# Kernel optimization log

Hardware: AMD Instinct MI355X
Metric: run time of the kernel (lower is better)

## Reference

```python
import jax, jax.numpy as jnp
import numpy as np

T, B, D = 2048, 4, 1024


def setup_inputs() -> dict:
    key = jax.random.key(0)
    ks = jax.random.split(key, 4)
    data = jax.random.normal(ks[0], (T, B, D), dtype=jnp.float32)
    W_qkv = jax.random.normal(ks[1], (D, 3 * D), dtype=jnp.float32) * 0.02
    b_qkv = jnp.zeros((3 * D,), dtype=jnp.float32)
    # torch stores pos_bias as [1,1,T,T]; bilinear interp to the same [T,T] size
    # (align_corners=False) is the identity, so we keep a [T,T] table directly.
    pos_bias_param = jax.random.normal(ks[2], (T, T), dtype=jnp.float32) * 0.02
    W_out = jax.random.normal(ks[3], (D, D), dtype=jnp.float32) * 0.02
    b_out = jnp.zeros((D,), dtype=jnp.float32)
    return {"data": data, "W_qkv": W_qkv, "b_qkv": b_qkv,
            "pos_bias_param": pos_bias_param, "W_out": W_out, "b_out": b_out}


def reference(data, W_qkv, b_qkv, pos_bias_param, W_out, b_out):
    # data: [T, B, D]
    qkv = data @ W_qkv + b_qkv                      # [T, B, 3D]
    q, k, v = jnp.split(qkv, 3, axis=-1)            # each [T, B, D]
    pb = pos_bias_param                             # [T, T] (i=query pos, j=key pos)
    max_key = jnp.max(k, axis=0, keepdims=True)     # [1, B, D]
    max_pb = jnp.max(pb, axis=1, keepdims=True)     # [T, 1]
    exp_key = jnp.exp(k - max_key)                  # [T, B, D]
    exp_pb = jnp.exp(pb - max_pb)                   # [T, T]
    # torch einsum 'ijb,jbd->ibd' with b=1 on pos_bias broadcasts -> plain ij contraction
    num = jnp.einsum('ij,jbd->ibd', exp_pb, exp_key * v)  # [T, B, D]
    den = jnp.einsum('ij,jbd->ibd', exp_pb, exp_key)       # [T, B, D]
    y = jax.nn.sigmoid(q) * num / den               # [T, B, D]
    return y @ W_out + b_out
```

## Files before the change

### kernel.cpp

```cpp
#include <hip/hip_runtime.h>
#include <stdint.h>

typedef unsigned short ushort_t;
typedef signed char s8;
typedef __attribute__((ext_vector_type(8))) short short8;
typedef __attribute__((ext_vector_type(4))) int int4v;
typedef __attribute__((ext_vector_type(4))) float float4v;

typedef const void __attribute__((address_space(1)))* gptr1_t;
typedef void __attribute__((address_space(3)))* lptr3_t;

#define SX   (5.5f/127.f)
#define ISX  (127.f/5.5f)
#define SW1  (0.11f/127.f)
#define ISW1 (127.f/0.11f)
#define S1   (SX*SW1)

static __device__ __forceinline__ ushort_t f2bf(float f) {
  unsigned u = __builtin_bit_cast(unsigned, f);
  u += 0x7fffu + ((u >> 16) & 1u);
  return (ushort_t)(u >> 16);
}
static __device__ __forceinline__ float bf2f(ushort_t h) {
  unsigned u = ((unsigned)h) << 16;
  return __builtin_bit_cast(float, u);
}
static __device__ __forceinline__ float frcp(float x) { return __builtin_amdgcn_rcpf(x); }
static __device__ __forceinline__ int q8(float x, float inv_s) {
  float v = fminf(fmaxf(x * inv_s, -127.f), 127.f);
  return (int)rintf(v);
}

__global__ __launch_bounds__(256)
void prep1(const float* __restrict__ data, s8* __restrict__ Xq,
           const float* __restrict__ Wqkv, s8* __restrict__ WqT) {
  __shared__ float t[32][33];
  const int blk = blockIdx.x, tid = threadIdx.x;
  if (blk < 8192) {
    int row = blk;
    int orow = (row & 3) * 2048 + (row >> 2);
    float4v v = ((const float4v*)(data + (size_t)row * 1024))[tid];
    int a0 = q8(v[0], ISX), a1 = q8(v[1], ISX), a2 = q8(v[2], ISX), a3 = q8(v[3], ISX);
    uint32_t p = (a0 & 255) | ((a1 & 255) << 8) | ((a2 & 255) << 16) | ((a3 & 255) << 24);
    ((uint32_t*)(Xq + (size_t)orow * 1024))[tid] = p;
  } else {
    int l = blk - 8192;
    int bx = l % 96, by = l / 96;
    int tx = tid & 31, ty = tid >> 5;
    int c = bx * 32 + tx;
    #pragma unroll
    for (int i = ty; i < 32; i += 8)
      t[i][tx] = Wqkv[(size_t)(by * 32 + i) * 3072 + c];
    __syncthreads();
    int r = by * 32 + tx;
    #pragma unroll
    for (int i = ty; i < 32; i += 8) {
      int orow = bx * 32 + i;
      orow = (orow < 1024) ? orow
           : (orow < 2048) ? 1024 + 2 * (orow - 1024)
                           : 1024 + 2 * (orow - 2048) + 1;
      WqT[(size_t)orow * 1024 + r] = (s8)q8(t[tx][i], ISW1);
    }
  }
}


#define FENCE() asm volatile("" ::: "memory")
#define BARRIER() do { FENCE(); __builtin_amdgcn_s_barrier(); FENCE(); } while (0)
#define SB() __builtin_amdgcn_sched_barrier(0)
#define WAIT_LGKM0() do { asm volatile("s_waitcnt lgkmcnt(0)" ::: "memory"); SB(); } while (0)
#define WAIT_LGKM8() do { asm volatile("s_waitcnt lgkmcnt(8)" ::: "memory"); SB(); } while (0)
#define WAIT_VM0()   do { asm volatile("s_waitcnt vmcnt(0)"   ::: "memory"); SB(); } while (0)

#define GLD(g, l) __builtin_amdgcn_global_load_lds((gptr1_t)(const void*)(g), \
                                                   (lptr3_t)(void*)(l), 16, 0, 0)

#define STAGEA(h, u, bb) do { \
  const char* gs_ = gA + (size_t)(h) * 128 * AROWB + (size_t)(u) * 128; \
  char* ls_ = Als + (bb) * 32768 + (((h) * 128 + wid * 16) << 7); \
  GLD(gs_, ls_); GLD(gs_ + 8 * AROWB, ls_ + 1024); \
} while (0)
#define STAGEB(h, u, bb) do { \
  const char* gs_ = gB + (size_t)(h) * 128 * BROWB + (size_t)(u) * 128; \
  char* ls_ = Bls + (bb) * 32768 + (((h) * 128 + wid * 16) << 7); \
  GLD(gs_, ls_); GLD(gs_ + 8 * BROWB, ls_ + 1024); \
} while (0)

#define STAGE4(gbase, lbase, tn, bb, ROWB) do { \
  const char* gs_ = (gbase) + (size_t)(tn) * 128; \
  char* ls_ = (lbase) + (bb) * 32768 + ((wid * 32) << 7); \
  GLD(gs_, ls_); GLD(gs_ + 8 * (size_t)(ROWB), ls_ + 1024); \
  GLD(gs_ + 16 * (size_t)(ROWB), ls_ + 2048); GLD(gs_ + 24 * (size_t)(ROWB), ls_ + 3072); \
} while (0)

#define LDA2(DST, p, bb) do { \
  const fragt* As_ = (const fragt*)(Als + (bb) * 32768); \
  _Pragma("unroll") \
  for (int ii_ = 0; ii_ < 2; ++ii_) { \
    const int row_ = arow + ((p) * 2 + ii_) * 16 + m16; \
    DST[ii_][0] = As_[row_ * 8 + (quad ^ swr)]; \
    DST[ii_][1] = As_[row_ * 8 + ((4 + quad) ^ swr)]; \
  } \
} while (0)
#define LDB2Q(DST, q, bb) do { \
  const fragt* Bs_ = (const fragt*)(Bls + (bb) * BSTRIDE); \
  _Pragma("unroll") \
  for (int jj_ = 0; jj_ < 2; ++jj_) { \
    const int row_ = brow + ((q) * 2 + jj_) * 16 + m16; \
    DST[jj_][0] = Bs_[row_ * 8 + (quad ^ swr)]; \
    DST[jj_][1] = Bs_[row_ * 8 + ((4 + quad) ^ swr)]; \
  } \
} while (0)

#define MM8(AF, BF, ib, jb) do { \
  __builtin_amdgcn_s_setprio(1); \
  _Pragma("unroll") \
  for (int ks_ = 0; ks_ < 2; ++ks_) \
    _Pragma("unroll") \
    for (int ii_ = 0; ii_ < 2; ++ii_) \
      _Pragma("unroll") \
      for (int jj_ = 0; jj_ < 2; ++jj_) \
        acc[(ib) + ii_][(jb) + jj_] = MFMA_OP( \
            AF[ii_][ks_], BF[jj_][ks_], acc[(ib) + ii_][(jb) + jj_]); \
  __builtin_amdgcn_s_setprio(0); \
  SB(); \
} while (0)

#define WAIT_LGKM4() do { asm volatile("s_waitcnt lgkmcnt(4)" ::: "memory"); SB(); } while (0)
#define TILE256_BODY(bb) \
  LDA2(afX, 0, bb); LDB2Q(bfQ0, 0, bb); SB(); \
  LDA2(afY, 1, bb); LDB2Q(bfQ1, 1, bb); SB(); \
  WAIT_LGKM8(); \
  MM8(afX, bfQ0, 0, 0); \
  WAIT_LGKM0(); \
  MM8(afX, bfQ1, 0, 2); \
  LDA2(afX, 2, bb); SB(); \
  MM8(afY, bfQ0, 2, 0); \
  MM8(afY, bfQ1, 2, 2); \
  LDA2(afY, 3, bb); SB(); \
  WAIT_LGKM4(); \
  MM8(afX, bfQ0, 4, 0); \
  MM8(afX, bfQ1, 4, 2); \
  WAIT_LGKM0(); \
  MM8(afY, bfQ0, 6, 0); \
  MM8(afY, bfQ1, 6, 2);

#define TILE256(bb, tn) do { \
  STAGEA(0, tn, (bb) ^ 1); STAGEA(1, tn, (bb) ^ 1); \
  STAGEB(0, tn, (bb) ^ 1); STAGEB(1, tn, (bb) ^ 1); \
  TILE256_BODY(bb) \
  WAIT_VM0(); \
  BARRIER(); \
} while (0)

#define TILE256_LAST(bb) do { TILE256_BODY(bb) } while (0)

#define MFMA_OP(a, b, c) __builtin_amdgcn_mfma_i32_16x16x64_i8(a, b, c, 0, 0, 0)
#define BSTRIDE 32768
__global__ __launch_bounds__(512, 2)
void g1mix(const s8* __restrict__ WqT, const s8* __restrict__ Xq,
           const float* __restrict__ bqkv,
           uint32_t* __restrict__ qP, ushort_t* __restrict__ GT,
           const float* __restrict__ pb, ushort_t* __restrict__ Pb,
           const float* __restrict__ Wout, ushort_t* __restrict__ WoT) {
  __shared__ __align__(16) char smem[131072];
  const int blk = blockIdx.x, tid = threadIdx.x;
  if (blk < 384) {
    typedef int4v fragt;
    const int wid  = tid >> 6;
    const int lane = tid & 63;
    const int wr = wid >> 2, wc = wid & 3;
    const int m16 = lane & 15, quad = lane >> 4;
    const int swr = m16 & 7;
    const int srow = lane >> 3, schk = lane & 7;
    const int arow = wr * 128, brow = wc * 64;

    const int wg = (blk & 7) * 48 + (blk >> 3);
    const int m0 = (wg >> 5) * 256;
    const int n0 = (wg & 31) * 256;

    int4v acc[8][4];
    #pragma unroll
    for (int i = 0; i < 8; ++i)
      #pragma unroll
      for (int j = 0; j < 4; ++j)
        #pragma unroll
        for (int r = 0; r < 4; ++r) acc[i][j][r] = 0;

    fragt afX[2][2], afY[2][2], bfQ0[2][2], bfQ1[2][2];

    const size_t AROWB = 1024, BROWB = 1024;
    const int colb = (schk ^ srow) * 16;
    const char* gA = (const char*)WqT + (size_t)(m0 + wid * 16 + srow) * 1024 + colb;
    const char* gB = (const char*)Xq  + (size_t)(n0 + wid * 16 + srow) * 1024 + colb;
    char* Als = smem;
    char* Bls = smem + 65536;

    STAGEA(0, 0, 0); STAGEA(1, 0, 0); STAGEB(0, 0, 0); STAGEB(1, 0, 0);
    WAIT_VM0();
    BARRIER();

    #pragma unroll 1
    for (int I = 0; I < 3; ++I) {
      TILE256(0, 2 * I + 1);
      TILE256(1, 2 * I + 2);
    }
    TILE256(0, 7);
    TILE256_LAST(1);

    if (m0 < 1024) {
      #pragma unroll
      for (int i = 0; i < 8; ++i)
        #pragma unroll
        for (int j = 0; j < 4; ++j) {
          const int gm = m0 + wr * 128 + i * 16 + quad * 4;
          const int gn = n0 + wc * 64 + j * 16 + m16;
          float f0 = (float)acc[i][j][0] * S1 + bqkv[gm];
          float f1 = (float)acc[i][j][1] * S1 + bqkv[gm + 1];
          float f2 = (float)acc[i][j][2] * S1 + bqkv[gm + 2];
          float f3 = (float)acc[i][j][3] * S1 + bqkv[gm + 3];
          qP[(size_t)(gm >> 1) * 8192 + gn]       = (uint32_t)f2bf(f0) | ((uint32_t)f2bf(f1) << 16);
          qP[(size_t)((gm >> 1) + 1) * 8192 + gn] = (uint32_t)f2bf(f2) | ((uint32_t)f2bf(f3) << 16);
        }
    } else {
      #pragma unroll
      for (int i = 0; i < 8; ++i)
        #pragma unroll
        for (int j = 0; j < 4; ++j) {
          const int gm = m0 + wr * 128 + i * 16 + quad * 4;
          const int gn = n0 + wc * 64 + j * 16 + m16;
          const int d  = (gm - 1024) >> 1;
          const int t  = gn & 2047, bb = gn >> 11;
          #pragma unroll
          for (int p = 0; p < 2; ++p) {
            float kk = (float)acc[i][j][2 * p]     * S1 + bqkv[1024 + d + p];
            float vv = (float)acc[i][j][2 * p + 1] * S1 + bqkv[2048 + d + p];
            float ek = __expf(kk);
            int c = bb * 1024 + d + p;
            GT[(size_t)(2 * c)     * 2048 + t] = f2bf(ek * vv);
            GT[(size_t)(2 * c + 1) * 2048 + t] = f2bf(ek);
          }
        }
    }
  } else if (blk < 640) {
    const int base = (blk - 384) * 4096;
    #pragma unroll
    for (int r = 0; r < 8; ++r) {
      int i = base + r * 512 + tid;
      float4v v = *(const float4v*)(pb + (size_t)i * 4);
      ushort_t o0 = f2bf(__expf(v[0])), o1 = f2bf(__expf(v[1]));
      ushort_t o2 = f2bf(__expf(v[2])), o3 = f2bf(__expf(v[3]));
      uint64_t p = (uint64_t)o0 | ((uint64_t)o1 << 16) | ((uint64_t)o2 << 32) | ((uint64_t)o3 << 48);
      *(uint64_t*)(Pb + (size_t)i * 4) = p;
    }
  } else {
    float (*t)[33] = (float (*)[33])smem;
    const int tx = tid & 31, ty = tid >> 5;
    #pragma unroll 1
    for (int rep = 0; rep < 8; ++rep) {
      int l = (blk - 640) * 8 + rep;
      int bx = l & 31, by = l >> 5;
      int c = bx * 32 + tx;
      #pragma unroll
      for (int i = ty; i < 32; i += 16)
        t[i][tx] = Wout[(size_t)(by * 32 + i) * 1024 + c];
      __syncthreads();
      int r = by * 32 + tx;
      #pragma unroll
      for (int i = ty; i < 32; i += 16)
        WoT[(size_t)(bx * 32 + i) * 1024 + r] = f2bf(t[tx][i]);
      __syncthreads();
    }
  }
}
#undef MFMA_OP
#undef BSTRIDE

#define MFMA_OP(a, b, c) __builtin_amdgcn_mfma_f32_16x16x32_bf16(a, b, c, 0, 0, 0)
#define BSTRIDE 16384
#define G3_STAGEB(tn, bb) do { \
  const char* gs_ = gB + (size_t)(tn) * 128; \
  char* ls_ = Bls + (bb) * 16384 + ((wid * 16) << 7); \
  GLD(gs_, ls_); GLD(gs_ + 8 * 2048, ls_ + 1024); \
} while (0)

#define G3_BODY(bb) \
  LDA2(afX, 0, bb); LDB2Q(bfQ0, 0, bb); SB(); \
  LDA2(afY, 1, bb); LDB2Q(bfQ1, 1, bb); SB(); \
  WAIT_LGKM8(); \
  MM8(afX, bfQ0, 0, 0); \
  WAIT_LGKM0(); \
  MM8(afX, bfQ1, 0, 2); \
  MM8(afY, bfQ0, 2, 0); \
  MM8(afY, bfQ1, 2, 2);

#define G3_TILE(bb, tn) do { \
  STAGE4(gA, Als, tn, (bb) ^ 1, 2048); \
  G3_STAGEB(tn, (bb) ^ 1); \
  G3_BODY(bb) \
  WAIT_VM0(); \
  BARRIER(); \
} while (0)

__global__ __launch_bounds__(512, 2)
void gemm3(const ushort_t* __restrict__ A, const ushort_t* __restrict__ BT,
           const float* __restrict__ bias, float* __restrict__ Cf) {
  __shared__ __align__(16) char smem[98304];
  typedef short8 fragt;
  const int tid  = threadIdx.x;
  const int wid  = tid >> 6;
  const int lane = tid & 63;
  const int wr = wid >> 1, wc = wid & 1;
  const int m16 = lane & 15, quad = lane >> 4;
  const int swr = m16 & 7;
  const int srow = lane >> 3, schk = lane & 7;
  const int arow = wr * 64, brow = wc * 64;

  const int bid = blockIdx.x;
  const int wg = (bid & 7) * 32 + (bid >> 3);
  const int m0 = (wg >> 3) * 256;
  const int n0 = (wg & 7) * 128;

  float4v acc[4][4];
  #pragma unroll
  for (int i = 0; i < 4; ++i)
    #pragma unroll
    for (int j = 0; j < 4; ++j)
      #pragma unroll
      for (int r = 0; r < 4; ++r) acc[i][j][r] = 0.0f;

  fragt afX[2][2], afY[2][2], bfQ0[2][2], bfQ1[2][2];

  const int colb = (schk ^ srow) * 16;
  const char* gA = (const char*)A  + (size_t)(m0 + wid * 32 + srow) * 2048 + colb;
  const char* gB = (const char*)BT + (size_t)(n0 + wid * 16 + srow) * 2048 + colb;
  char* Als = smem;
  char* Bls = smem + 65536;

  STAGE4(gA, Als, 0, 0, 2048);
  G3_STAGEB(0, 0);
  WAIT_VM0();
  BARRIER();

  #pragma unroll 1
  for (int I = 0; I < 7; ++I) {
    G3_TILE(0, 2 * I + 1);
    G3_TILE(1, 2 * I + 2);
  }
  G3_TILE(0, 15);
  G3_BODY(1)

  #pragma unroll
  for (int i = 0; i < 4; ++i)
    #pragma unroll
    for (int j = 0; j < 4; ++j) {
      const int gm = m0 + wr * 64 + i * 16 + quad * 4;
      const int gn = n0 + wc * 64 + j * 16 + m16;
      const float bv = bias[gn];
      #pragma unroll
      for (int r = 0; r < 4; ++r)
        Cf[(size_t)(gm + r) * 1024 + gn] = acc[i][j][r] + bv;
    }
}
#undef MFMA_OP
#undef BSTRIDE

#define MFMA_OP(a, b, c) __builtin_amdgcn_mfma_f32_16x16x32_bf16(a, b, c, 0, 0, 0)
#define BSTRIDE 32768
__global__ __launch_bounds__(512, 2)
void aft256(const ushort_t* __restrict__ A, const ushort_t* __restrict__ BT,
            ushort_t* __restrict__ Yb, const uint32_t* __restrict__ qP) {
  __shared__ __align__(16) char smem[131072];
  typedef short8 fragt;
  const int tid  = threadIdx.x;
  const int wid  = tid >> 6;
  const int lane = tid & 63;
  const int wr = wid >> 2, wc = wid & 3;
  const int m16 = lane & 15, quad = lane >> 4;
  const int swr = m16 & 7;
  const int srow = lane >> 3, schk = lane & 7;
  const int arow = wr * 128, brow = wc * 64;

  const int bid = blockIdx.x;
  const int wg = (bid & 7) * 32 + (bid >> 3);
  const int m0 = (wg >> 3) * 256;
  const int n0 = (wg & 7) * 256;

  float4v acc[8][4];
  #pragma unroll
  for (int i = 0; i < 8; ++i)
    #pragma unroll
    for (int j = 0; j < 4; ++j)
      #pragma unroll
      for (int r = 0; r < 4; ++r) acc[i][j][r] = 0.0f;

  fragt afX[2][2], afY[2][2], bfQ0[2][2], bfQ1[2][2];

  const size_t AROWB = 4096, BROWB = 4096;
  const int colb = (schk ^ srow) * 16;
  const char* gA = (const char*)A  + (size_t)(m0 + wid * 16 + srow) * 4096 + colb;
  const char* gB = (const char*)BT + (size_t)(n0 + wid * 16 + srow) * 4096 + colb;
  char* Als = smem;
  char* Bls = smem + 65536;

  STAGEA(0, 0, 0); STAGEA(1, 0, 0); STAGEB(0, 0, 0); STAGEB(1, 0, 0);
  WAIT_VM0();
  BARRIER();

  #pragma unroll 1
  for (int I = 0; I < 15; ++I) {
    TILE256(0, 2 * I + 1);
    TILE256(1, 2 * I + 2);
  }
  TILE256(0, 31);
  TILE256_LAST(1);

  __syncthreads();

  uint32_t* tb = (uint32_t*)smem;
  const int cbase = m0 >> 1;
  const int b = cbase >> 10, dbase = cbase & 1023;
  const int pbase = dbase >> 1;
  #pragma unroll
  for (int i = 0; i < 8; ++i) {
    const int wl = wr * 32 + i * 4 + quad;
    #pragma unroll
    for (int j = 0; j < 4; ++j) {
      const int tl = wc * 64 + j * 16 + m16;
      const int t  = n0 + tl;
      uint32_t qw = qP[(size_t)(pbase + wl) * 8192 + b * 2048 + t];
      float q0 = bf2f((ushort_t)(qw & 0xffffu));
      float q1 = bf2f((ushort_t)(qw >> 16));
      float y0 = frcp(1.0f + __expf(-q0)) * acc[i][j][0] * frcp(acc[i][j][1]);
      float y1 = frcp(1.0f + __expf(-q1)) * acc[i][j][2] * frcp(acc[i][j][3]);
      tb[tl * 65 + wl] = (uint32_t)f2bf(y0) | ((uint32_t)f2bf(y1) << 16);
    }
  }
  __syncthreads();
  uint32_t* Yw = (uint32_t*)Yb;
  const int lw = tid & 63, trow = tid >> 6;
  #pragma unroll
  for (int it = 0; it < 32; ++it) {
    const int tl = it * 8 + trow;
    const int t  = n0 + tl;
    Yw[(size_t)(4 * t + b) * 512 + (dbase >> 1) + lw] = tb[tl * 65 + lw];
  }
}
#undef MFMA_OP
#undef BSTRIDE


extern "C" void kernel_launch(void* const* d_in, const int* in_sizes, int n_in,
                              void* d_out, int out_size, void* d_ws, size_t ws_size,
                              hipStream_t stream) {
  const float* data = (const float*)d_in[0];
  const float* Wqkv = (const float*)d_in[1];
  const float* bqkv = (const float*)d_in[2];
  const float* pb   = (const float*)d_in[3];
  const float* Wout = (const float*)d_in[4];
  const float* bout = (const float*)d_in[5];
  float* out = (float*)d_out;

  char* ws = (char*)d_ws;
  s8*       Xq  = (s8*)(ws);
  s8*       WqT = (s8*)(ws + (8ull  << 20));
  ushort_t* WoT = (ushort_t*)(ws + (11ull << 20));
  ushort_t* Pb  = (ushort_t*)(ws + (13ull << 20));
  uint32_t* qPw = (uint32_t*)(ws + (21ull << 20));
  ushort_t* GT  = (ushort_t*)(ws + (37ull << 20));
  ushort_t* Y   = (ushort_t*)(ws + (69ull << 20));

  prep1<<<11264, 256, 0, stream>>>(data, Xq, Wqkv, WqT);
  g1mix<<<768, 512, 0, stream>>>(WqT, Xq, bqkv, qPw, GT, pb, Pb, Wout, WoT);
  aft256<<<256, 512, 0, stream>>>(GT, Pb, Y, qPw);
  gemm3<<<256, 512, 0, stream>>>(Y, WoT, bout, out);
}
```

Before: 226.7 us.

## Interleave LDS fragment reads, global prefetch and MFMAs per k-chunk in 256-tile GEMMs

Replaces the 256x256 tile body used by the int8 QKV GEMM and the bf16 AFT GEMM with a finer software pipeline. LDS fragment reads are now split per k-chunk, and the next tile's global-to-LDS loads are spread between MFMA groups instead of all being issued up front. Waits use graded lgkmcnt thresholds. The goal is to overlap LDS latency and global prefetch with matrix-core work, at the cost of more fragile manual waitcnt scheduling and different register pressure.

```diff
diff --git a/kernel.cpp b/kernel.cpp
--- a/kernel.cpp
+++ b/kernel.cpp
@@ -69,6 +69,9 @@
 #define BARRIER() do { FENCE(); __builtin_amdgcn_s_barrier(); FENCE(); } while (0)
 #define SB() __builtin_amdgcn_sched_barrier(0)
 #define WAIT_LGKM0() do { asm volatile("s_waitcnt lgkmcnt(0)" ::: "memory"); SB(); } while (0)
+#define WAIT_LGKM2() do { asm volatile("s_waitcnt lgkmcnt(2)" ::: "memory"); SB(); } while (0)
+#define WAIT_LGKM4() do { asm volatile("s_waitcnt lgkmcnt(4)" ::: "memory"); SB(); } while (0)
+#define WAIT_LGKM6() do { asm volatile("s_waitcnt lgkmcnt(6)" ::: "memory"); SB(); } while (0)
 #define WAIT_LGKM8() do { asm volatile("s_waitcnt lgkmcnt(8)" ::: "memory"); SB(); } while (0)
 #define WAIT_VM0()   do { asm volatile("s_waitcnt vmcnt(0)"   ::: "memory"); SB(); } while (0)
 
@@ -93,70 +96,73 @@
   GLD(gs_ + 16 * (size_t)(ROWB), ls_ + 2048); GLD(gs_ + 24 * (size_t)(ROWB), ls_ + 3072); \
 } while (0)
 
-#define LDA2(DST, p, bb) do { \
+#define RA2(p, kc, bb) do { \
   const fragt* As_ = (const fragt*)(Als + (bb) * 32768); \
-  _Pragma("unroll") \
-  for (int ii_ = 0; ii_ < 2; ++ii_) { \
-    const int row_ = arow + ((p) * 2 + ii_) * 16 + m16; \
-    DST[ii_][0] = As_[row_ * 8 + (quad ^ swr)]; \
-    DST[ii_][1] = As_[row_ * 8 + ((4 + quad) ^ swr)]; \
-  } \
-} while (0)
-#define LDB2Q(DST, q, bb) do { \
-  const fragt* Bs_ = (const fragt*)(Bls + (bb) * BSTRIDE); \
-  _Pragma("unroll") \
-  for (int jj_ = 0; jj_ < 2; ++jj_) { \
-    const int row_ = brow + ((q) * 2 + jj_) * 16 + m16; \
-    DST[jj_][0] = Bs_[row_ * 8 + (quad ^ swr)]; \
-    DST[jj_][1] = Bs_[row_ * 8 + ((4 + quad) ^ swr)]; \
-  } \
-} while (0)
-
-#define MM8(AF, BF, ib, jb) do { \
+  af[p][0] = As_[(arow + ((p) * 2 + 0) * 16 + m16) * 8 + (((kc) * 4 + quad) ^ swr)]; \
+  af[p][1] = As_[(arow + ((p) * 2 + 1) * 16 + m16) * 8 + (((kc) * 4 + quad) ^ swr)]; \
+  SB(); \
+} while (0)
+#define RB2(q, kc, bb) do { \
+  const fragt* Bs_ = (const fragt*)(Bls + (bb) * 32768); \
+  bq[q][kc][0] = Bs_[(brow + ((q) * 2 + 0) * 16 + m16) * 8 + (((kc) * 4 + quad) ^ swr)]; \
+  bq[q][kc][1] = Bs_[(brow + ((q) * 2 + 1) * 16 + m16) * 8 + (((kc) * 4 + quad) ^ swr)]; \
+  SB(); \
+} while (0)
+
+#define MM4(p, q, kc) do { \
   __builtin_amdgcn_s_setprio(1); \
-  _Pragma("unroll") \
-  for (int ks_ = 0; ks_ < 2; ++ks_) \
-    _Pragma("unroll") \
-    for (int ii_ = 0; ii_ < 2; ++ii_) \
-      _Pragma("unroll") \
-      for (int jj_ = 0; jj_ < 2; ++jj_) \
-        acc[(ib) + ii_][(jb) + jj_] = MFMA_OP( \
-            AF[ii_][ks_], BF[jj_][ks_], acc[(ib) + ii_][(jb) + jj_]); \
+  acc[(p)*2+0][(q)*2+0] = MFMA_OP(af[p][0], bq[q][kc][0], acc[(p)*2+0][(q)*2+0]); \
+  acc[(p)*2+1][(q)*2+0] = MFMA_OP(af[p][1], bq[q][kc][0], acc[(p)*2+1][(q)*2+0]); \
+  acc[(p)*2+0][(q)*2+1] = MFMA_OP(af[p][0], bq[q][kc][1], acc[(p)*2+0][(q)*2+1]); \
+  acc[(p)*2+1][(q)*2+1] = MFMA_OP(af[p][1], bq[q][kc][1], acc[(p)*2+1][(q)*2+1]); \
   __builtin_amdgcn_s_setprio(0); \
   SB(); \
 } while (0)
 
-#define WAIT_LGKM4() do { asm volatile("s_waitcnt lgkmcnt(4)" ::: "memory"); SB(); } while (0)
-#define TILE256_BODY(bb) \
-  LDA2(afX, 0, bb); LDB2Q(bfQ0, 0, bb); SB(); \
-  LDA2(afY, 1, bb); LDB2Q(bfQ1, 1, bb); SB(); \
-  WAIT_LGKM8(); \
-  MM8(afX, bfQ0, 0, 0); \
-  WAIT_LGKM0(); \
-  MM8(afX, bfQ1, 0, 2); \
-  LDA2(afX, 2, bb); SB(); \
-  MM8(afY, bfQ0, 2, 0); \
-  MM8(afY, bfQ1, 2, 2); \
-  LDA2(afY, 3, bb); SB(); \
-  WAIT_LGKM4(); \
-  MM8(afX, bfQ0, 4, 0); \
-  MM8(afX, bfQ1, 4, 2); \
-  WAIT_LGKM0(); \
-  MM8(afY, bfQ0, 6, 0); \
-  MM8(afY, bfQ1, 6, 2);
-
-#define TILE256(bb, tn) do { \
-  STAGEA(0, tn, (bb) ^ 1); STAGEA(1, tn, (bb) ^ 1); \
-  STAGEB(0, tn, (bb) ^ 1); STAGEB(1, tn, (bb) ^ 1); \
-  TILE256_BODY(bb) \
+#define TILEP(bb, tn) do { \
+  RA2(0, 0, bb); RB2(0, 0, bb); \
+  STAGEA(0, tn, (bb) ^ 1); \
+  RA2(1, 0, bb); RB2(1, 0, bb); \
+  WAIT_LGKM4(); MM4(0, 0, 0); \
+  RA2(2, 0, bb); \
+  STAGEA(1, tn, (bb) ^ 1); STAGEB(0, tn, (bb) ^ 1); \
+  WAIT_LGKM2(); MM4(1, 0, 0); MM4(0, 1, 0); MM4(1, 1, 0); \
+  RA2(3, 0, bb); RA2(0, 1, bb); RB2(0, 1, bb); \
+  WAIT_LGKM6(); MM4(2, 0, 0); \
+  STAGEB(1, tn, (bb) ^ 1); \
+  RB2(1, 1, bb); \
+  WAIT_LGKM6(); MM4(3, 0, 0); MM4(2, 1, 0); MM4(3, 1, 0); \
+  RA2(1, 1, bb); \
+  WAIT_LGKM4(); MM4(0, 0, 1); \
+  RA2(2, 1, bb); \
+  WAIT_LGKM2(); MM4(1, 0, 1); MM4(0, 1, 1); MM4(1, 1, 1); \
+  RA2(3, 1, bb); \
+  WAIT_LGKM2(); MM4(2, 0, 1); \
+  WAIT_LGKM0(); MM4(3, 0, 1); MM4(2, 1, 1); MM4(3, 1, 1); \
   WAIT_VM0(); \
   BARRIER(); \
 } while (0)
 
-#define TILE256_LAST(bb) do { TILE256_BODY(bb) } while (0)
+#define TILEP_LAST(bb) do { \
+  RA2(0, 0, bb); RB2(0, 0, bb); \
+  RA2(1, 0, bb); RB2(1, 0, bb); \
+  WAIT_LGKM4(); MM4(0, 0, 0); \
+  RA2(2, 0, bb); \
+  WAIT_LGKM2(); MM4(1, 0, 0); MM4(0, 1, 0); MM4(1, 1, 0); \
+  RA2(3, 0, bb); RA2(0, 1, bb); RB2(0, 1, bb); \
+  WAIT_LGKM6(); MM4(2, 0, 0); \
+  RB2(1, 1, bb); \
+  WAIT_LGKM6(); MM4(3, 0, 0); MM4(2, 1, 0); MM4(3, 1, 0); \
+  RA2(1, 1, bb); \
+  WAIT_LGKM4(); MM4(0, 0, 1); \
+  RA2(2, 1, bb); \
+  WAIT_LGKM2(); MM4(1, 0, 1); MM4(0, 1, 1); MM4(1, 1, 1); \
+  RA2(3, 1, bb); \
+  WAIT_LGKM2(); MM4(2, 0, 1); \
+  WAIT_LGKM0(); MM4(3, 0, 1); MM4(2, 1, 1); MM4(3, 1, 1); \
+} while (0)
 
 #define MFMA_OP(a, b, c) __builtin_amdgcn_mfma_i32_16x16x64_i8(a, b, c, 0, 0, 0)
-#define BSTRIDE 32768
 __global__ __launch_bounds__(512, 2)
 void g1mix(const s8* __restrict__ WqT, const s8* __restrict__ Xq,
            const float* __restrict__ bqkv,
@@ -187,7 +193,7 @@
         #pragma unroll
         for (int r = 0; r < 4; ++r) acc[i][j][r] = 0;
 
-    fragt afX[2][2], afY[2][2], bfQ0[2][2], bfQ1[2][2];
+    fragt af[4][2], bq[2][2][2];
 
     const size_t AROWB = 1024, BROWB = 1024;
     const int colb = (schk ^ srow) * 16;
@@ -202,11 +208,11 @@
 
     #pragma unroll 1
     for (int I = 0; I < 3; ++I) {
-      TILE256(0, 2 * I + 1);
-      TILE256(1, 2 * I + 2);
-    }
-    TILE256(0, 7);
-    TILE256_LAST(1);
+      TILEP(0, 2 * I + 1);
+      TILEP(1, 2 * I + 2);
+    }
+    TILEP(0, 7);
+    TILEP_LAST(1);
 
     if (m0 < 1024) {
       #pragma unroll
@@ -274,10 +280,41 @@
   }
 }
 #undef MFMA_OP
-#undef BSTRIDE
+
+#define BSTRIDE 16384
+#define LDA2(DST, p, bb) do { \
+  const fragt* As_ = (const fragt*)(Als + (bb) * 32768); \
+  _Pragma("unroll") \
+  for (int ii_ = 0; ii_ < 2; ++ii_) { \
+    const int row_ = arow + ((p) * 2 + ii_) * 16 + m16; \
+    DST[ii_][0] = As_[row_ * 8 + (quad ^ swr)]; \
+    DST[ii_][1] = As_[row_ * 8 + ((4 + quad) ^ swr)]; \
+  } \
+} while (0)
+#define LDB2Q(DST, q, bb) do { \
+  const fragt* Bs_ = (const fragt*)(Bls + (bb) * BSTRIDE); \
+  _Pragma("unroll") \
+  for (int jj_ = 0; jj_ < 2; ++jj_) { \
+    const int row_ = brow + ((q) * 2 + jj_) * 16 + m16; \
+    DST[jj_][0] = Bs_[row_ * 8 + (quad ^ swr)]; \
+    DST[jj_][1] = Bs_[row_ * 8 + ((4 + quad) ^ swr)]; \
+  } \
+} while (0)
+#define MM8(AF, BF, ib, jb) do { \
+  __builtin_amdgcn_s_setprio(1); \
+  _Pragma("unroll") \
+  for (int ks_ = 0; ks_ < 2; ++ks_) \
+    _Pragma("unroll") \
+    for (int ii_ = 0; ii_ < 2; ++ii_) \
+      _Pragma("unroll") \
+      for (int jj_ = 0; jj_ < 2; ++jj_) \
+        acc[(ib) + ii_][(jb) + jj_] = MFMA_OP( \
+            AF[ii_][ks_], BF[jj_][ks_], acc[(ib) + ii_][(jb) + jj_]); \
+  __builtin_amdgcn_s_setprio(0); \
+  SB(); \
+} while (0)
 
 #define MFMA_OP(a, b, c) __builtin_amdgcn_mfma_f32_16x16x32_bf16(a, b, c, 0, 0, 0)
-#define BSTRIDE 16384
 #define G3_STAGEB(tn, bb) do { \
   const char* gs_ = gB + (size_t)(tn) * 128; \
   char* ls_ = Bls + (bb) * 16384 + ((wid * 16) << 7); \
@@ -366,7 +403,6 @@
 #undef BSTRIDE
 
 #define MFMA_OP(a, b, c) __builtin_amdgcn_mfma_f32_16x16x32_bf16(a, b, c, 0, 0, 0)
-#define BSTRIDE 32768
 __global__ __launch_bounds__(512, 2)
 void aft256(const ushort_t* __restrict__ A, const ushort_t* __restrict__ BT,
             ushort_t* __restrict__ Yb, const uint32_t* __restrict__ qP) {
@@ -394,7 +430,7 @@
       #pragma unroll
       for (int r = 0; r < 4; ++r) acc[i][j][r] = 0.0f;
 
-  fragt afX[2][2], afY[2][2], bfQ0[2][2], bfQ1[2][2];
+  fragt af[4][2], bq[2][2][2];
 
   const size_t AROWB = 4096, BROWB = 4096;
   const int colb = (schk ^ srow) * 16;
@@ -409,11 +445,11 @@
 
   #pragma unroll 1
   for (int I = 0; I < 15; ++I) {
-    TILE256(0, 2 * I + 1);
-    TILE256(1, 2 * I + 2);
+    TILEP(0, 2 * I + 1);
+    TILEP(1, 2 * I + 2);
   }
-  TILE256(0, 31);
-  TILE256_LAST(1);
+  TILEP(0, 31);
+  TILEP_LAST(1);
 
   __syncthreads();
 
@@ -447,7 +483,6 @@
   }
 }
 #undef MFMA_OP
-#undef BSTRIDE
 
 
 extern "C" void kernel_launch(void* const* d_in, const int* in_sizes, int n_in,
```

New measurement: 217.9 us. -3.9%, faster.
